# Optimization experiments

Measured on AMD Instinct MI355X. Metric: run time of the kernel, lower is better.

## Reference

```python
import jax, jax.numpy as jnp
import numpy as np

B, N, F_, D = 4, 1024, 10, 16
DOUT = 16
EMB = 10  # nn.LayerNorm(10)
NF = N * F_


def setup_inputs() -> dict:
    key = jax.random.key(0)
    ks = jax.random.split(key, 8)
    x = jax.random.normal(ks[0], (B, N, F_, D), dtype=jnp.float32)
    factor_embeddings = jax.random.normal(ks[1], (F_, EMB), dtype=jnp.float32)
    grid_embeddings = jax.random.normal(ks[2], (N, EMB), dtype=jnp.float32)
    supports = jax.random.uniform(ks[3], (NF, NF), dtype=jnp.float32)
    # parameters
    ln_gamma = jnp.ones((EMB,), jnp.float32)
    ln_beta = jnp.zeros((EMB,), jnp.float32)
    W_gcn = jax.random.normal(ks[4], (D, DOUT), dtype=jnp.float32) * 0.05
    b_gcn = jnp.zeros((DOUT,), jnp.float32)
    W_out = jax.random.normal(ks[5], (F_ * DOUT, DOUT), dtype=jnp.float32) * 0.05
    b_out = jnp.zeros((DOUT,), jnp.float32)
    return {"x": x, "factor_embeddings": factor_embeddings,
            "grid_embeddings": grid_embeddings, "supports": supports,
            "ln_gamma": ln_gamma, "ln_beta": ln_beta,
            "W_gcn": W_gcn, "b_gcn": b_gcn, "W_out": W_out, "b_out": b_out}


def _layernorm(h, g, b, eps=1e-12):
    mu = jnp.mean(h, axis=-1, keepdims=True)
    var = jnp.mean(jnp.square(h - mu), axis=-1, keepdims=True)
    return (h - mu) / jnp.sqrt(var + eps) * g + b


def reference(x, factor_embeddings, grid_embeddings, supports,
              ln_gamma, ln_beta, W_gcn, b_gcn, W_out, b_out):
    b_, n_, f_, d_ = x.shape
    nf = n_ * f_
    xf = x.reshape(b_, nf, d_)

    # --- factor-graph attention (DEAD CODE in the original forward: the
    # masked factor_graphs tensor is never used; dense_to_sparse reads
    # `supports` directly). Computed here for shape fidelity only. ---
    gfe = _layernorm(factor_embeddings[None, :, :] + grid_embeddings[:, None, :],
                     ln_gamma, ln_beta)               # (N, F, EMB)
    factor_graphs = jax.nn.softmax(jnp.einsum('nfd,ngd->nfg', gfe, gfe), axis=-1)
    _ = factor_graphs  # the (NF,NF) repeat * supports is unused -> omitted

    # --- GCNConv(normalize=True) on the dense-to-sparse(supports) graph ---
    # add_remaining_self_loops: keep existing diag weights, fill zeros with 1
    diag = jnp.diagonal(supports)
    idx = jnp.arange(nf)
    A = supports.at[idx, idx].set(jnp.where(diag == 0, 1.0, diag))
    deg = A.sum(axis=0)                               # scatter_add over col (target)
    dinv = jnp.where(deg > 0, jax.lax.rsqrt(deg), 0.0)
    A_norm = dinv[:, None] * A * dinv[None, :]        # norm_ij = d_i^-1/2 A_ij d_j^-1/2

    h = jnp.einsum('bid,do->bio', xf, W_gcn)          # GCN linear (no bias)
    h = jnp.einsum('ij,bio->bjo', A_norm, h) + b_gcn  # aggregate src i -> dst j
    h = jax.nn.relu(h)                                # (B, NF, DOUT)

    h = h.reshape(b_, n_, f_ * h.shape[-1])           # (B, N, F*DOUT)
    return h @ W_out + b_out                          # (B, N, DOUT)
```

## Files before the change

### kernel.cpp

```cpp
#include <hip/hip_runtime.h>
#include <cstdint>
#include <cstddef>

#define NF 10240

typedef _Float16 half8_t __attribute__((ext_vector_type(8)));
typedef _Float16 half4_t __attribute__((ext_vector_type(4)));
typedef float floatx4 __attribute__((ext_vector_type(4)));

__global__ __launch_bounds__(256) void k_prep(const float* __restrict__ sup,
                                              _Float16* __restrict__ Ah,
                                              float* __restrict__ deg) {
  __shared__ float lsum[8 * 128];
  const int t = threadIdx.x;
  const int j0 = blockIdx.x * 128;
  const int i0 = blockIdx.y * 320;
  const int cq = t & 31;
  const int rg = t >> 5;
  const int j = j0 + cq * 4;
  float4 s4 = {0.f, 0.f, 0.f, 0.f};
  const bool diagBlock = (i0 < j0 + 128) && (j0 < i0 + 320);
#pragma unroll 4
  for (int p = 0; p < 40; ++p) {
    const int i = i0 + p * 8 + rg;
    float4 v = *(const float4*)(sup + (size_t)i * NF + j);
    if (diagBlock) {
      if (i == j     && v.x == 0.f) v.x = 1.f;
      if (i == j + 1 && v.y == 0.f) v.y = 1.f;
      if (i == j + 2 && v.z == 0.f) v.z = 1.f;
      if (i == j + 3 && v.w == 0.f) v.w = 1.f;
    }
    s4.x += v.x; s4.y += v.y; s4.z += v.z; s4.w += v.w;
    half4_t h;
    h[0] = (_Float16)v.x; h[1] = (_Float16)v.y;
    h[2] = (_Float16)v.z; h[3] = (_Float16)v.w;
    *(half4_t*)(Ah + (size_t)i * NF + j) = h;
  }
  lsum[rg * 128 + cq * 4 + 0] = s4.x;
  lsum[rg * 128 + cq * 4 + 1] = s4.y;
  lsum[rg * 128 + cq * 4 + 2] = s4.z;
  lsum[rg * 128 + cq * 4 + 3] = s4.w;
  __syncthreads();
  if (t < 128) {
    float s = 0.f;
#pragma unroll
    for (int r = 0; r < 8; ++r) s += lsum[r * 128 + t];
    atomicAdd(&deg[j0 + t], s);
  }
}

__global__ __launch_bounds__(256) void k_g(const float* __restrict__ x,
                                           const float* __restrict__ Wg,
                                           const float* __restrict__ deg,
                                           float* __restrict__ dinv,
                                           _Float16* __restrict__ gp) {
  __shared__ float w[256];
  w[threadIdx.x] = Wg[threadIdx.x];
  __syncthreads();
  const int t = blockIdx.x * 256 + threadIdx.x;
  const int b = t / NF;
  const int i = t % NF;
  float xv[16];
  const float* xp = x + (size_t)t * 16;
#pragma unroll
  for (int d = 0; d < 16; ++d) xv[d] = xp[d];
  const float dg = deg[i];
  const float di = dg > 0.f ? rsqrtf(dg) : 0.f;
  if (b == 0) dinv[i] = di;
  const int base = ((i >> 3) * 64 + b * 16) * 8 + (i & 7);
#pragma unroll
  for (int o = 0; o < 16; ++o) {
    float h = 0.f;
#pragma unroll
    for (int d = 0; d < 16; ++d) h += xv[d] * w[d * 16 + o];
    gp[base + o * 8] = (_Float16)(h * di);
  }
}

__global__ __launch_bounds__(256) void k_gemm2(const _Float16* __restrict__ Ah,
                                               const half8_t* __restrict__ gp8,
                                               float* __restrict__ Cp,
                                               int kRange, int nchunk) {
  __shared__ unsigned int lds32[64 * 36];
  const int tid = threadIdx.x;
  const int lane = tid & 63;
  const int w = tid >> 6;
  const int x = lane & 15;
  const int q = lane >> 4;
  const int jbase = blockIdx.x * 64;
  const int kbase0 = blockIdx.y * kRange;
  const int cq = tid & 15;
  const int ip = tid >> 4;

  floatx4 acc[4] = {};

  for (int ch = 0; ch < nchunk; ++ch) {
    const int kbase = kbase0 + ch * 64;
    __syncthreads();
#pragma unroll
    for (int p = 0; p < 2; ++p) {
      const int il = p * 32 + ip * 2;
      const _Float16* r0 = Ah + (size_t)(kbase + il) * NF + jbase + cq * 4;
      const ushort4 a0 = *(const ushort4*)r0;
      const ushort4 a1 = *(const ushort4*)(r0 + NF);
      unsigned int* d = &lds32[(cq * 4) * 36 + p * 16 + ip];
      d[0]   = (unsigned)a0.x | ((unsigned)a1.x << 16);
      d[36]  = (unsigned)a0.y | ((unsigned)a1.y << 16);
      d[72]  = (unsigned)a0.z | ((unsigned)a1.z << 16);
      d[108] = (unsigned)a0.w | ((unsigned)a1.w << 16);
    }
    __syncthreads();
    const int k8base = kbase >> 3;
#pragma unroll
    for (int s = 0; s < 2; ++s) {
      const half8_t bfrag = gp8[(k8base + s * 4 + q) * 64 + w * 16 + x];
#pragma unroll
      for (int ms = 0; ms < 4; ++ms) {
        const half8_t afrag = *(const half8_t*)((const _Float16*)lds32 +
                                (ms * 16 + x) * 72 + s * 32 + q * 8);
        acc[ms] = __builtin_amdgcn_mfma_f32_16x16x32_f16(afrag, bfrag,
                                                         acc[ms], 0, 0, 0);
      }
    }
  }

  const size_t pbase = (size_t)blockIdx.y * NF;
#pragma unroll
  for (int ms = 0; ms < 4; ++ms) {
#pragma unroll
    for (int r = 0; r < 4; ++r) {
      const int j = jbase + ms * 16 + q * 4 + r;
      Cp[(pbase + j) * 64 + w * 16 + x] = acc[ms][r];
    }
  }
}

__global__ __launch_bounds__(256) void k_out(const float* __restrict__ Cp,
                                             const float* __restrict__ dinv,
                                             const float* __restrict__ bgcn,
                                             const float* __restrict__ Wout,
                                             const float* __restrict__ bout,
                                             float* __restrict__ out, int S) {
  __shared__ float wl[2560];
  __shared__ float tmp[640];
  const int n = blockIdx.x;
  const int t = threadIdx.x;
  for (int idx = t; idx < 2560; idx += 256) wl[idx] = Wout[idx];
  if (t < 160) {
    const int f = t >> 4, o = t & 15;
    const int j = n * 10 + f;
    const float di = dinv[j];
    const float bg = bgcn[o];
    for (int b = 0; b < 4; ++b) {
      float s = 0.f;
      for (int p = 0; p < S; ++p)
        s += Cp[((size_t)(p * NF + j)) * 64 + b * 16 + o];
      const float v = di * s + bg;
      tmp[b * 160 + t] = v > 0.f ? v : 0.f;
    }
  }
  __syncthreads();
  if (t < 64) {
    const int b = t >> 4, oc = t & 15;
    float acc = bout[oc];
    for (int k = 0; k < 160; ++k) acc += tmp[b * 160 + k] * wl[k * 16 + oc];
    out[((size_t)(b * 1024 + n)) * 16 + oc] = acc;
  }
}

extern "C" void kernel_launch(void* const* d_in, const int* in_sizes, int n_in,
                              void* d_out, int out_size, void* d_ws,
                              size_t ws_size, hipStream_t stream) {
  const float* x   = (const float*)d_in[0];
  const float* sup = (const float*)d_in[3];
  const float* Wg  = (const float*)d_in[6];
  const float* bg  = (const float*)d_in[7];
  const float* Wo  = (const float*)d_in[8];
  const float* bo  = (const float*)d_in[9];
  float* out = (float*)d_out;

  char* ws = (char*)d_ws;
  float*     deg  = (float*)ws;
  float*     dinv = (float*)(ws + 40960);
  _Float16*  gp   = (_Float16*)(ws + 81920);
  _Float16*  Ah   = (_Float16*)(ws + 1392640);
  float*     Cp   = (float*)(ws + 1392640 + 209715200);

  const int S = 8;
  const int kRange = NF / S;
  const int nchunk = kRange / 64;

  hipMemsetAsync(deg, 0, NF * sizeof(float), stream);
  k_prep<<<dim3(80, 32), 256, 0, stream>>>(sup, Ah, deg);
  k_g<<<160, 256, 0, stream>>>(x, Wg, deg, dinv, gp);
  k_gemm2<<<dim3(160, S), 256, 0, stream>>>(Ah, (const half8_t*)gp, Cp,
                                            kRange, nchunk);
  k_out<<<1024, 256, 0, stream>>>(Cp, dinv, bg, Wo, bo, out, S);
}
```

Before: 676.7 us.

## Replace degree atomics with partial sums, widen GEMM K-chunk, coalesce split-K output

```diff
diff --git a/kernel.cpp b/kernel.cpp
--- a/kernel.cpp
+++ b/kernel.cpp
@@ -7,51 +7,49 @@
 typedef _Float16 half8_t __attribute__((ext_vector_type(8)));
 typedef _Float16 half4_t __attribute__((ext_vector_type(4)));
 typedef float floatx4 __attribute__((ext_vector_type(4)));
+typedef float fvec4 __attribute__((ext_vector_type(4)));
 
 __global__ __launch_bounds__(256) void k_prep(const float* __restrict__ sup,
                                               _Float16* __restrict__ Ah,
-                                              float* __restrict__ deg) {
-  __shared__ float lsum[8 * 128];
+                                              float* __restrict__ degP) {
+  __shared__ float lsum[4 * 256];
   const int t = threadIdx.x;
-  const int j0 = blockIdx.x * 128;
+  const int j0 = blockIdx.x * 256;
   const int i0 = blockIdx.y * 320;
-  const int cq = t & 31;
-  const int rg = t >> 5;
-  const int j = j0 + cq * 4;
-  float4 s4 = {0.f, 0.f, 0.f, 0.f};
-  const bool diagBlock = (i0 < j0 + 128) && (j0 < i0 + 320);
+  const int cj = t & 63;
+  const int rg = t >> 6;
+  const int j = j0 + cj * 4;
+  fvec4 s4 = {0.f, 0.f, 0.f, 0.f};
+  const bool diagBlock = (i0 < j0 + 256) && (j0 < i0 + 320);
 #pragma unroll 4
-  for (int p = 0; p < 40; ++p) {
-    const int i = i0 + p * 8 + rg;
-    float4 v = *(const float4*)(sup + (size_t)i * NF + j);
+  for (int p = 0; p < 80; ++p) {
+    const int i = i0 + p * 4 + rg;
+    const fvec4* src = (const fvec4*)(sup + (size_t)i * NF + j);
+    fvec4 v = __builtin_nontemporal_load(src);
     if (diagBlock) {
       if (i == j     && v.x == 0.f) v.x = 1.f;
       if (i == j + 1 && v.y == 0.f) v.y = 1.f;
       if (i == j + 2 && v.z == 0.f) v.z = 1.f;
       if (i == j + 3 && v.w == 0.f) v.w = 1.f;
     }
-    s4.x += v.x; s4.y += v.y; s4.z += v.z; s4.w += v.w;
+    s4 += v;
     half4_t h;
     h[0] = (_Float16)v.x; h[1] = (_Float16)v.y;
     h[2] = (_Float16)v.z; h[3] = (_Float16)v.w;
     *(half4_t*)(Ah + (size_t)i * NF + j) = h;
   }
-  lsum[rg * 128 + cq * 4 + 0] = s4.x;
-  lsum[rg * 128 + cq * 4 + 1] = s4.y;
-  lsum[rg * 128 + cq * 4 + 2] = s4.z;
-  lsum[rg * 128 + cq * 4 + 3] = s4.w;
-  __syncthreads();
-  if (t < 128) {
-    float s = 0.f;
-#pragma unroll
-    for (int r = 0; r < 8; ++r) s += lsum[r * 128 + t];
-    atomicAdd(&deg[j0 + t], s);
-  }
+  lsum[rg * 256 + cj * 4 + 0] = s4.x;
+  lsum[rg * 256 + cj * 4 + 1] = s4.y;
+  lsum[rg * 256 + cj * 4 + 2] = s4.z;
+  lsum[rg * 256 + cj * 4 + 3] = s4.w;
+  __syncthreads();
+  float s = lsum[t] + lsum[256 + t] + lsum[512 + t] + lsum[768 + t];
+  degP[(size_t)blockIdx.y * NF + j0 + t] = s;
 }
 
 __global__ __launch_bounds__(256) void k_g(const float* __restrict__ x,
                                            const float* __restrict__ Wg,
-                                           const float* __restrict__ deg,
+                                           const float* __restrict__ degP,
                                            float* __restrict__ dinv,
                                            _Float16* __restrict__ gp) {
   __shared__ float w[256];
@@ -60,11 +58,13 @@
   const int t = blockIdx.x * 256 + threadIdx.x;
   const int b = t / NF;
   const int i = t % NF;
+  float dg = 0.f;
+#pragma unroll 8
+  for (int c = 0; c < 32; ++c) dg += degP[(size_t)c * NF + i];
   float xv[16];
   const float* xp = x + (size_t)t * 16;
 #pragma unroll
   for (int d = 0; d < 16; ++d) xv[d] = xp[d];
-  const float dg = deg[i];
   const float di = dg > 0.f ? rsqrtf(dg) : 0.f;
   if (b == 0) dinv[i] = di;
   const int base = ((i >> 3) * 64 + b * 16) * 8 + (i & 7);
@@ -77,11 +77,11 @@
   }
 }
 
-__global__ __launch_bounds__(256) void k_gemm2(const _Float16* __restrict__ Ah,
+__global__ __launch_bounds__(256) void k_gemm3(const _Float16* __restrict__ Ah,
                                                const half8_t* __restrict__ gp8,
                                                float* __restrict__ Cp,
                                                int kRange, int nchunk) {
-  __shared__ unsigned int lds32[64 * 36];
+  __shared__ unsigned int lds32[64 * 68];
   const int tid = threadIdx.x;
   const int lane = tid & 63;
   const int w = tid >> 6;
@@ -95,42 +95,42 @@
   floatx4 acc[4] = {};
 
   for (int ch = 0; ch < nchunk; ++ch) {
-    const int kbase = kbase0 + ch * 64;
+    const int kbase = kbase0 + ch * 128;
     __syncthreads();
 #pragma unroll
-    for (int p = 0; p < 2; ++p) {
+    for (int p = 0; p < 4; ++p) {
       const int il = p * 32 + ip * 2;
       const _Float16* r0 = Ah + (size_t)(kbase + il) * NF + jbase + cq * 4;
       const ushort4 a0 = *(const ushort4*)r0;
       const ushort4 a1 = *(const ushort4*)(r0 + NF);
-      unsigned int* d = &lds32[(cq * 4) * 36 + p * 16 + ip];
+      unsigned int* d = &lds32[(cq * 4) * 68 + p * 16 + ip];
       d[0]   = (unsigned)a0.x | ((unsigned)a1.x << 16);
-      d[36]  = (unsigned)a0.y | ((unsigned)a1.y << 16);
-      d[72]  = (unsigned)a0.z | ((unsigned)a1.z << 16);
-      d[108] = (unsigned)a0.w | ((unsigned)a1.w << 16);
+      d[68]  = (unsigned)a0.y | ((unsigned)a1.y << 16);
+      d[136] = (unsigned)a0.z | ((unsigned)a1.z << 16);
+      d[204] = (unsigned)a0.w | ((unsigned)a1.w << 16);
     }
     __syncthreads();
     const int k8base = kbase >> 3;
 #pragma unroll
-    for (int s = 0; s < 2; ++s) {
+    for (int s = 0; s < 4; ++s) {
       const half8_t bfrag = gp8[(k8base + s * 4 + q) * 64 + w * 16 + x];
 #pragma unroll
       for (int ms = 0; ms < 4; ++ms) {
         const half8_t afrag = *(const half8_t*)((const _Float16*)lds32 +
-                                (ms * 16 + x) * 72 + s * 32 + q * 8);
+                                (ms * 16 + x) * 136 + s * 32 + q * 8);
         acc[ms] = __builtin_amdgcn_mfma_f32_16x16x32_f16(afrag, bfrag,
                                                          acc[ms], 0, 0, 0);
       }
     }
   }
 
-  const size_t pbase = (size_t)blockIdx.y * NF;
+  const int p = blockIdx.y;
 #pragma unroll
   for (int ms = 0; ms < 4; ++ms) {
 #pragma unroll
     for (int r = 0; r < 4; ++r) {
       const int j = jbase + ms * 16 + q * 4 + r;
-      Cp[(pbase + j) * 64 + w * 16 + x] = acc[ms][r];
+      Cp[((size_t)j * 8 + p) * 64 + w * 16 + x] = acc[ms][r];
     }
   }
 }
@@ -140,21 +140,33 @@
                                              const float* __restrict__ bgcn,
                                              const float* __restrict__ Wout,
                                              const float* __restrict__ bout,
-                                             float* __restrict__ out, int S) {
+                                             float* __restrict__ out) {
   __shared__ float wl[2560];
+  __shared__ float cps[5120];
   __shared__ float tmp[640];
   const int n = blockIdx.x;
   const int t = threadIdx.x;
-  for (int idx = t; idx < 2560; idx += 256) wl[idx] = Wout[idx];
+  {
+    const float4* src = (const float4*)(Cp + (size_t)n * 5120);
+    float4* dst = (float4*)cps;
+#pragma unroll
+    for (int r = 0; r < 5; ++r) dst[t + r * 256] = src[t + r * 256];
+    const float4* ws = (const float4*)Wout;
+    float4* wd = (float4*)wl;
+#pragma unroll
+    for (int r = 0; r < 2; ++r) wd[t + r * 256] = ws[t + r * 256];
+    if (t < 128) wd[512 + t] = ws[512 + t];
+  }
+  __syncthreads();
   if (t < 160) {
     const int f = t >> 4, o = t & 15;
-    const int j = n * 10 + f;
-    const float di = dinv[j];
+    const float di = dinv[n * 10 + f];
     const float bg = bgcn[o];
+#pragma unroll
     for (int b = 0; b < 4; ++b) {
       float s = 0.f;
-      for (int p = 0; p < S; ++p)
-        s += Cp[((size_t)(p * NF + j)) * 64 + b * 16 + o];
+#pragma unroll
+      for (int p = 0; p < 8; ++p) s += cps[(f * 8 + p) * 64 + b * 16 + o];
       const float v = di * s + bg;
       tmp[b * 160 + t] = v > 0.f ? v : 0.f;
     }
@@ -180,20 +192,19 @@
   float* out = (float*)d_out;
 
   char* ws = (char*)d_ws;
-  float*     deg  = (float*)ws;
-  float*     dinv = (float*)(ws + 40960);
-  _Float16*  gp   = (_Float16*)(ws + 81920);
-  _Float16*  Ah   = (_Float16*)(ws + 1392640);
-  float*     Cp   = (float*)(ws + 1392640 + 209715200);
+  float*     degP = (float*)ws;
+  float*     dinv = (float*)(ws + 1310720);
+  _Float16*  gp   = (_Float16*)(ws + 1351680);
+  _Float16*  Ah   = (_Float16*)(ws + 2662400);
+  float*     Cp   = (float*)(ws + 2662400 + 209715200);
 
   const int S = 8;
   const int kRange = NF / S;
-  const int nchunk = kRange / 64;
-
-  hipMemsetAsync(deg, 0, NF * sizeof(float), stream);
-  k_prep<<<dim3(80, 32), 256, 0, stream>>>(sup, Ah, deg);
-  k_g<<<160, 256, 0, stream>>>(x, Wg, deg, dinv, gp);
-  k_gemm2<<<dim3(160, S), 256, 0, stream>>>(Ah, (const half8_t*)gp, Cp,
+  const int nchunk = kRange / 128;
+
+  k_prep<<<dim3(40, 32), 256, 0, stream>>>(sup, Ah, degP);
+  k_g<<<160, 256, 0, stream>>>(x, Wg, degP, dinv, gp);
+  k_gemm3<<<dim3(160, S), 256, 0, stream>>>(Ah, (const half8_t*)gp, Cp,
                                             kRange, nchunk);
-  k_out<<<1024, 256, 0, stream>>>(Cp, dinv, bg, Wo, bo, out, S);
-}
+  k_out<<<1024, 256, 0, stream>>>(Cp, dinv, bg, Wo, bo, out);
+}
```

Result: faster. 636.8 us (-5.9%).
